# Performance work log

Hardware: AMD Instinct MI355X
Metric: run time of the kernel (lower is better)

## Reference

```python
import jax, jax.numpy as jnp
import numpy as np

IN_C, OUT_C, K, STRIDE, PAD, N_EXPERTS = 64, 128, 3, 1, 1, 4
B, H, W = 32, 64, 64


def setup_inputs() -> dict:
    key = jax.random.key(0)
    k1, k2, k3, k4 = jax.random.split(key, 4)
    x = jax.random.normal(k1, (B, IN_C, H, W), dtype=jnp.float32)
    idx = jax.random.randint(k2, (B,), 0, N_EXPERTS, dtype=jnp.int64)
    # Expert conv weights/biases (PyTorch Conv2d layout: [out_c, in_c, kh, kw])
    fan_in = IN_C * K * K
    bound = 1.0 / np.sqrt(fan_in)
    Wc = jax.random.uniform(k3, (N_EXPERTS, OUT_C, IN_C, K, K), dtype=jnp.float32,
                            minval=-bound, maxval=bound)
    bc = jax.random.uniform(k4, (N_EXPERTS, OUT_C), dtype=jnp.float32,
                            minval=-bound, maxval=bound)
    return {"x": x, "idx": idx, "Wc": Wc, "bc": bc}


def _conv2d(x, w, b):
    # x: [B, C_in, H, W], w: [C_out, C_in, K, K], b: [C_out]
    y = jax.lax.conv_general_dilated(
        x, w,
        window_strides=(STRIDE, STRIDE),
        padding=[(PAD, PAD), (PAD, PAD)],
        dimension_numbers=("NCHW", "OIHW", "NCHW"),
    )
    return y + b[None, :, None, None]


def reference(x, idx, Wc, bc):
    # Compute every expert's conv for every sample (faithful to the torch code),
    # then gather each sample's selected expert output.
    results = jax.vmap(lambda w, b: _conv2d(x, w, b))(Wc, bc)  # [E, B, C_out, H, W]
    results = jnp.moveaxis(results, 0, 1)                      # [B, E, C_out, H, W]
    out = jnp.take_along_axis(
        results, idx[:, None, None, None, None].astype(jnp.int32), axis=1
    )  # [B, 1, C_out, H, W]
    return jnp.squeeze(out, axis=1)
```

## Files before the change

kernel.cpp:

```cpp
#include <hip/hip_runtime.h>
#include <hip/hip_bf16.h>


#define IC 64
#define OC 128
#define HH 64
#define WW 64

typedef short short8 __attribute__((ext_vector_type(8)));
typedef ushort ushort8 __attribute__((ext_vector_type(8)));
typedef float float16 __attribute__((ext_vector_type(16)));

static __device__ __forceinline__ ushort f2bf(float v) {
    __hip_bfloat16 h = __float2bfloat16(v);
    return *(ushort*)&h;
}

__global__ __launch_bounds__(256)
void reorder_w(const float* __restrict__ Wc, ushort* __restrict__ wout) {
    __shared__ ushort lw[4 * 584];
    const int t   = threadIdx.x;
    const int e   = blockIdx.x >> 5;
    const int oc0 = (blockIdx.x & 31) * 4;
    const float* src = Wc + (size_t)(e * 128 + oc0) * 576;
#pragma unroll
    for (int k = 0; k < 9; ++k) {
        const int f   = k * 256 + t;
        const int ocl = f / 576;
        const int rem = f - ocl * 576;
        lw[ocl * 584 + rem] = f2bf(src[f]);
    }
    __syncthreads();
#pragma unroll
    for (int k = 0; k < 2; ++k) {
        const int n = k * 256 + t;
        if (n < 288) {
            const int ocl = n & 3, ich = (n >> 2) & 7, tap = n >> 5;
            ushort8 v;
#pragma unroll
            for (int icl = 0; icl < 8; ++icl)
                v[icl] = lw[ocl * 584 + (ich * 8 + icl) * 9 + tap];
            *(ushort8*)(wout +
                ((((size_t)(e * 9 + tap) * 8 + ich) * 128 + oc0 + ocl) * 8)) = v;
        }
    }
}

__global__ __launch_bounds__(256, 4)
void moe_conv_mfma(const float* __restrict__ x, const int* __restrict__ idx,
                   const ushort* __restrict__ wre, const float* __restrict__ bc,
                   float* __restrict__ out) {
    __shared__ __align__(16) ushort xs[4 * 8 * 66 * 8];
    __shared__ float bias[128];

    const int t = threadIdx.x;

    const int lin = blockIdx.x;
    const int nw  = (lin & 7) * 128 + (lin >> 3);
    const int b   = nw >> 5;
    const int rp  = nw & 31;
    const int row0 = rp * 2;
    const int e    = ((unsigned)idx[b]) & 3;

    const int lane31 = t & 31;
    const int lhi    = (t >> 5) & 1;
    const int wv     = t >> 6;
    const int w0     = wv & 1;
    const int pr     = wv >> 1;

    const ushort* wsrc = wre + (size_t)e * 9 * 8192
                       + ((size_t)lhi * 128 + w0 * 64 + lane31) * 8;

    short8 a0c = *(const short8*)(wsrc);
    short8 a1c = *(const short8*)(wsrc + 256);

    if (t < 128) {
        const int r = t >> 5, rem = t & 31;
        const int ich = rem >> 2, side = (rem >> 1) & 1, q = rem & 1;
        const int hc = side ? 65 : 0;
        ushort4 z = {0, 0, 0, 0};
        *(ushort4*)&xs[(((r * 8 + ich) * 66 + hc) * 8 + q * 4)] = z;
    } else {
        bias[t - 128] = bc[e * OC + (t - 128)];
    }

    const float* xb = x + (size_t)b * IC * HH * WW;
    {
        const int gc   = t & 63;
        const int csel = t >> 6;
#pragma unroll
        for (int it = 0; it < 16; ++it) {
            const int combo = it * 4 + csel;
            const int r = combo >> 4, rem = combo & 15;
            const int ich = rem >> 1, q = rem & 1;
            const int gr = row0 - 1 + r;
            ushort4 u = {0, 0, 0, 0};
            if ((unsigned)gr < (unsigned)HH) {
                const int ic0 = ich * 8 + q * 4;
                u.x = f2bf(xb[((ic0 + 0) * HH + gr) * WW + gc]);
                u.y = f2bf(xb[((ic0 + 1) * HH + gr) * WW + gc]);
                u.z = f2bf(xb[((ic0 + 2) * HH + gr) * WW + gc]);
                u.w = f2bf(xb[((ic0 + 3) * HH + gr) * WW + gc]);
            }
            *(ushort4*)&xs[(((r * 8 + ich) * 66 + (gc + 1)) * 8 + q * 4)] = u;
        }
    }

    float16 acc[2][2];
#pragma unroll
    for (int a = 0; a < 2; ++a)
#pragma unroll
        for (int cg = 0; cg < 2; ++cg)
#pragma unroll
            for (int r = 0; r < 16; ++r) acc[a][cg][r] = 0.0f;

    __syncthreads();

    const int xbase = ((pr * 8 + lhi) * 66 + lane31) * 8;

#pragma unroll
    for (int s = 0; s < 36; ++s) {
        const int tap = s >> 2, ks = s & 3;
        const int kh  = tap / 3, kw = tap - kh * 3;
        const int off = ((kh * 8 + ks * 2) * 66 + kw) * 8;

        const short8 b0 = *(const short8*)&xs[xbase + off];
        const short8 b1 = *(const short8*)&xs[xbase + off + 256];

        short8 a0n, a1n;
        if (s < 35) {
            a0n = *(const short8*)(wsrc + (s + 1) * 2048);
            a1n = *(const short8*)(wsrc + (s + 1) * 2048 + 256);
        }

        __builtin_amdgcn_s_setprio(1);
        acc[0][0] = __builtin_amdgcn_mfma_f32_32x32x16_bf16(a0c, b0, acc[0][0], 0, 0, 0);
        acc[0][1] = __builtin_amdgcn_mfma_f32_32x32x16_bf16(a0c, b1, acc[0][1], 0, 0, 0);
        acc[1][0] = __builtin_amdgcn_mfma_f32_32x32x16_bf16(a1c, b0, acc[1][0], 0, 0, 0);
        acc[1][1] = __builtin_amdgcn_mfma_f32_32x32x16_bf16(a1c, b1, acc[1][1], 0, 0, 0);
        __builtin_amdgcn_s_setprio(0);

        if (s < 35) { a0c = a0n; a1c = a1n; }
    }

#pragma unroll
    for (int a = 0; a < 2; ++a) {
        const int ocb = w0 * 64 + a * 32 + 4 * lhi;
#pragma unroll
        for (int reg = 0; reg < 16; ++reg) {
            const int oc = ocb + (reg & 3) + 8 * (reg >> 2);
            const float bv = bias[oc];
            const size_t base = (((size_t)b * OC + oc) * HH + (row0 + pr)) * WW;
            out[base + lane31]      = acc[a][0][reg] + bv;
            out[base + 32 + lane31] = acc[a][1][reg] + bv;
        }
    }
}

extern "C" void kernel_launch(void* const* d_in, const int* in_sizes, int n_in,
                              void* d_out, int out_size, void* d_ws, size_t ws_size,
                              hipStream_t stream) {
    const float* x   = (const float*)d_in[0];
    const int*   idx = (const int*)d_in[1];
    const float* Wc  = (const float*)d_in[2];
    const float* bc  = (const float*)d_in[3];
    float* out  = (float*)d_out;
    ushort* wre = (ushort*)d_ws;

    reorder_w<<<128, 256, 0, stream>>>(Wc, wre);
    moe_conv_mfma<<<1024, 256, 0, stream>>>(x, idx, wre, bc, out);
}
```

Measured before the change: 112.5 us.

## Stage expert weights in double-buffered LDS via global_load_lds per tap

Replaces the per-wave register loads of the weight fragments from global memory with cooperative global_load_lds copies of each tap's 8192-element weight slice into a double-buffered shared array. The loop now runs per tap, prefetching the next tap while computing the current one, with barriers around each stage. The aim is to cut redundant global weight traffic across waves and hide its latency. In exchange it adds 32KB of LDS per block, which may reduce occupancy, plus two barriers per tap.

Measured after the change: 120.0 us. 6.7% more time.

```diff
diff --git a/kernel.cpp b/kernel.cpp
--- a/kernel.cpp
+++ b/kernel.cpp
@@ -10,6 +10,9 @@
 typedef short short8 __attribute__((ext_vector_type(8)));
 typedef ushort ushort8 __attribute__((ext_vector_type(8)));
 typedef float float16 __attribute__((ext_vector_type(16)));
+
+typedef const __attribute__((address_space(1))) void gas_t;
+typedef __attribute__((address_space(3))) void las_t;
 
 static __device__ __forceinline__ ushort f2bf(float v) {
     __hip_bfloat16 h = __float2bfloat16(v);
@@ -51,6 +54,7 @@
                    const ushort* __restrict__ wre, const float* __restrict__ bc,
                    float* __restrict__ out) {
     __shared__ __align__(16) ushort xs[4 * 8 * 66 * 8];
+    __shared__ __align__(16) ushort wbuf[2][8192];
     __shared__ float bias[128];
 
     const int t = threadIdx.x;
@@ -63,16 +67,20 @@
     const int e    = ((unsigned)idx[b]) & 3;
 
     const int lane31 = t & 31;
+    const int lane64 = t & 63;
     const int lhi    = (t >> 5) & 1;
     const int wv     = t >> 6;
     const int w0     = wv & 1;
     const int pr     = wv >> 1;
 
-    const ushort* wsrc = wre + (size_t)e * 9 * 8192
-                       + ((size_t)lhi * 128 + w0 * 64 + lane31) * 8;
+    const ushort* we = wre + (size_t)e * 9 * 8192;
 
-    short8 a0c = *(const short8*)(wsrc);
-    short8 a1c = *(const short8*)(wsrc + 256);
+#pragma unroll
+    for (int i = 0; i < 4; ++i) {
+        __builtin_amdgcn_global_load_lds(
+            (gas_t*)(we + wv * 2048 + i * 512 + lane64 * 8),
+            (las_t*)&wbuf[0][wv * 2048 + i * 512], 16, 0, 0);
+    }
 
     if (t < 128) {
         const int r = t >> 5, rem = t & 31;
@@ -114,33 +122,45 @@
 #pragma unroll
             for (int r = 0; r < 16; ++r) acc[a][cg][r] = 0.0f;
 
-    __syncthreads();
-
     const int xbase = ((pr * 8 + lhi) * 66 + lane31) * 8;
 
 #pragma unroll
-    for (int s = 0; s < 36; ++s) {
-        const int tap = s >> 2, ks = s & 3;
-        const int kh  = tap / 3, kw = tap - kh * 3;
-        const int off = ((kh * 8 + ks * 2) * 66 + kw) * 8;
+    for (int tap = 0; tap < 9; ++tap) {
+        const int cur = tap & 1;
+        if (tap < 8) {
+            const ushort* wt = we + (tap + 1) * 8192;
+#pragma unroll
+            for (int i = 0; i < 4; ++i) {
+                __builtin_amdgcn_global_load_lds(
+                    (gas_t*)(wt + wv * 2048 + i * 512 + lane64 * 8),
+                    (las_t*)&wbuf[cur ^ 1][wv * 2048 + i * 512], 16, 0, 0);
+            }
+            asm volatile("s_waitcnt vmcnt(4) lgkmcnt(0)" ::: "memory");
+        } else {
+            asm volatile("s_waitcnt vmcnt(0) lgkmcnt(0)" ::: "memory");
+        }
+        __builtin_amdgcn_s_barrier();
 
-        const short8 b0 = *(const short8*)&xs[xbase + off];
-        const short8 b1 = *(const short8*)&xs[xbase + off + 256];
-
-        short8 a0n, a1n;
-        if (s < 35) {
-            a0n = *(const short8*)(wsrc + (s + 1) * 2048);
-            a1n = *(const short8*)(wsrc + (s + 1) * 2048 + 256);
-        }
+        const int kh = tap / 3;
+        const int kw = tap - kh * 3;
+        const int off = ((kh * 8) * 66 + kw) * 8;
 
         __builtin_amdgcn_s_setprio(1);
-        acc[0][0] = __builtin_amdgcn_mfma_f32_32x32x16_bf16(a0c, b0, acc[0][0], 0, 0, 0);
-        acc[0][1] = __builtin_amdgcn_mfma_f32_32x32x16_bf16(a0c, b1, acc[0][1], 0, 0, 0);
-        acc[1][0] = __builtin_amdgcn_mfma_f32_32x32x16_bf16(a1c, b0, acc[1][0], 0, 0, 0);
-        acc[1][1] = __builtin_amdgcn_mfma_f32_32x32x16_bf16(a1c, b1, acc[1][1], 0, 0, 0);
+#pragma unroll
+        for (int ks = 0; ks < 4; ++ks) {
+            const int ich = ks * 2 + lhi;
+            const short8 a0 = *(const short8*)&wbuf[cur][(ich * 128 + w0 * 64 + lane31) * 8];
+            const short8 a1 = *(const short8*)&wbuf[cur][(ich * 128 + w0 * 64 + 32 + lane31) * 8];
+            const short8 b0 = *(const short8*)&xs[xbase + off + ks * 2 * 66 * 8];
+            const short8 b1 = *(const short8*)&xs[xbase + off + ks * 2 * 66 * 8 + 256];
+            acc[0][0] = __builtin_amdgcn_mfma_f32_32x32x16_bf16(a0, b0, acc[0][0], 0, 0, 0);
+            acc[0][1] = __builtin_amdgcn_mfma_f32_32x32x16_bf16(a0, b1, acc[0][1], 0, 0, 0);
+            acc[1][0] = __builtin_amdgcn_mfma_f32_32x32x16_bf16(a1, b0, acc[1][0], 0, 0, 0);
+            acc[1][1] = __builtin_amdgcn_mfma_f32_32x32x16_bf16(a1, b1, acc[1][1], 0, 0, 0);
+        }
         __builtin_amdgcn_s_setprio(0);
 
-        if (s < 35) { a0c = a0n; a1c = a1n; }
+        __builtin_amdgcn_s_barrier();
     }
 
 #pragma unroll
```
